# Kernel tuning notes

Measured on AMD Instinct MI355X. Metric: run time of the kernel, lower is better.

## Reference

```python
import jax, jax.numpy as jnp
import numpy as np

DIM = 768
NUM_HEADS = 12
HEAD_DIM = DIM // NUM_HEADS
SCALE = HEAD_DIM ** -0.5
RPB_HIDDEN = 64


def setup_inputs() -> dict:
    key = jax.random.key(0)
    ks = jax.random.split(key, 7)
    B, N, C = 8, 1024, DIM
    x = jax.random.normal(ks[0], (B, N, C), dtype=jnp.float32)
    qkv_w = jax.random.normal(ks[1], (3 * C, C), dtype=jnp.float32) * (C ** -0.5)
    proj_w = jax.random.normal(ks[2], (C, C), dtype=jnp.float32) * (C ** -0.5)
    proj_b = jnp.zeros((C,), dtype=jnp.float32)
    rpb_w1 = jax.random.normal(ks[3], (RPB_HIDDEN, 2), dtype=jnp.float32) * 0.5
    rpb_b1 = jax.random.normal(ks[4], (RPB_HIDDEN,), dtype=jnp.float32) * 0.1
    rpb_w2 = jax.random.normal(ks[5], (NUM_HEADS, RPB_HIDDEN), dtype=jnp.float32) * 0.1
    rpb_b2 = jax.random.normal(ks[6], (NUM_HEADS,), dtype=jnp.float32) * 0.1
    return {"x": x, "qkv_w": qkv_w, "proj_w": proj_w, "proj_b": proj_b,
            "rpb_w1": rpb_w1, "rpb_b1": rpb_b1, "rpb_w2": rpb_w2, "rpb_b2": rpb_b2}


def _relative_position_bias(N, w1, b1, w2, b2):
    # grid coords: x varies fastest, y varies slowest (perfect-square N assumed)
    g = int(N ** 0.5)
    c = jnp.arange(g, dtype=jnp.float32)
    cx = jnp.tile(c, g)                      # [N]
    cy = jnp.repeat(c, g)                    # [N]
    rel_x = cx[:, None] - cx[None, :]        # [N, N]
    rel_y = cy[:, None] - cy[None, :]        # [N, N]
    rel = jnp.stack([rel_x, rel_y], axis=-1) # [N, N, 2]
    h = jax.nn.relu(jnp.einsum('nmk,hk->nmh', rel, w1) + b1)    # [N, N, hidden]
    bias = jnp.einsum('nmk,hk->nmh', h, w2) + b2                # [N, N, H]
    return jnp.transpose(bias, (2, 0, 1))                       # [H, N, N]


def reference(x, qkv_w, proj_w, proj_b, rpb_w1, rpb_b1, rpb_w2, rpb_b2):
    B, N, C = x.shape
    H, D = NUM_HEADS, HEAD_DIM
    qkv = jnp.einsum('bnc,oc->bno', x, qkv_w)            # [B, N, 3C]
    qkv = qkv.reshape(B, N, 3, H, D).transpose(2, 0, 3, 1, 4)  # [3, B, H, N, D]
    q, k, v = qkv[0], qkv[1], qkv[2]
    attn = jnp.einsum('bhnd,bhmd->bhnm', q, k) * SCALE   # [B, H, N, N]
    bias = _relative_position_bias(N, rpb_w1, rpb_b1, rpb_w2, rpb_b2)
    attn = attn + bias[None]                              # broadcast over batch
    attn = jax.nn.softmax(attn, axis=-1)
    out = jnp.einsum('bhnm,bhmd->bhnd', attn, v)         # [B, H, N, D]
    out = out.transpose(0, 2, 1, 3).reshape(B, N, C)
    return jnp.einsum('bnc,oc->bno', out, proj_w) + proj_b
```

## Files before the change

### kernel.cpp

```cpp
#include <hip/hip_runtime.h>

#define C_DIM 768
#define NHEADS 12
#define HDIM 64
#define BATCH 8
#define SEQ 1024
#define SCALE_F 0.125f
#define TBL 3969
#define BTSL 2079

typedef float f32x4 __attribute__((ext_vector_type(4)));
typedef short s16x4 __attribute__((ext_vector_type(4)));
typedef short s16x8 __attribute__((ext_vector_type(8)));
typedef unsigned int u32x2 __attribute__((ext_vector_type(2)));

__device__ inline unsigned short f2bf(float f) {
    unsigned r;
    asm("v_cvt_pk_bf16_f32 %0, %1, %2" : "=v"(r) : "v"(f), "v"(f));
    return (unsigned short)r;
}
__device__ inline unsigned cvtpk(float lo, float hi) {
    unsigned r;
    asm("v_cvt_pk_bf16_f32 %0, %1, %2" : "=v"(r) : "v"(lo), "v"(hi));
    return r;
}

#define GLOAD_LDS16(gsrc, ldst)                                                   \
    __builtin_amdgcn_global_load_lds(                                             \
        (const __attribute__((address_space(1))) unsigned int*)(gsrc),            \
        (__attribute__((address_space(3))) unsigned int*)(ldst), 16, 0, 0)


__global__ __launch_bounds__(256)
void cvt_bf16_kernel(const float* __restrict__ in, unsigned short* __restrict__ out,
                     int n8)
{
    int i = blockIdx.x * 256 + threadIdx.x;
    if (i >= n8) return;
    const float4* p = (const float4*)in + (size_t)i * 2;
    float4 a = p[0], b = p[1];
    s16x8 v;
    v[0] = (short)f2bf(a.x); v[1] = (short)f2bf(a.y);
    v[2] = (short)f2bf(a.z); v[3] = (short)f2bf(a.w);
    v[4] = (short)f2bf(b.x); v[5] = (short)f2bf(b.y);
    v[6] = (short)f2bf(b.z); v[7] = (short)f2bf(b.w);
    *((s16x8*)out + i) = v;
}


#define MFMA_SWAP(aa, bb)                                          \
    _Pragma("unroll") for (int i_ = 0; i_ < 4; ++i_)               \
    _Pragma("unroll") for (int j_ = 0; j_ < 4; ++j_)               \
        acc[i_][j_] = __builtin_amdgcn_mfma_f32_16x16x32_bf16(     \
            bb[j_], aa[i_], acc[i_][j_], 0, 0, 0);

#define MFMA_NORM(aa, bb)                                          \
    _Pragma("unroll") for (int i_ = 0; i_ < 4; ++i_)               \
    _Pragma("unroll") for (int j_ = 0; j_ < 4; ++j_)               \
        acc[i_][j_] = __builtin_amdgcn_mfma_f32_16x16x32_bf16(     \
            aa[i_], bb[j_], acc[i_][j_], 0, 0, 0);

#define STG_HALF(buf, kt, half)                                                    \
    GLOAD_LDS16(Ab + ((size_t)(m0 + w * 32 + (half) * 16 + srow8) * 768 +          \
                (kt) * 64) * 2 + sch8 * 16, &Al[buf][w * 32 + (half) * 16][0]);    \
    GLOAD_LDS16(Ab + ((size_t)(m0 + w * 32 + (half) * 16 + 8 + srow8) * 768 +      \
                (kt) * 64) * 2 + sch8 * 16, &Al[buf][w * 32 + (half) * 16 + 8][0]);\
    GLOAD_LDS16(Wb + ((size_t)(n0 + w * 16 + (half) * 8 + srow8) * 768 +           \
                (kt) * 64) * 2 + sch8 * 16, &Bl[buf][w * 16 + (half) * 8][0]);

#define PHASE_READS(cur, s, ar, br)                                                \
    _Pragma("unroll") for (int i_ = 0; i_ < 4; ++i_) {                             \
        ar[i_] = *(const s16x8*)((const char*)&Al[cur][wr * 64 + i_ * 16 + l15][0] \
                 + ((((s) * 4 + lhi) ^ (l15 & 7)) * 16));                          \
        br[i_] = *(const s16x8*)((const char*)&Bl[cur][wc * 64 + i_ * 16 + l15][0] \
                 + ((((s) * 4 + lhi) ^ (l15 & 7)) * 16));                          \
    }

__global__ __launch_bounds__(512)
void gemm_qkv_mfma(const unsigned short* __restrict__ A,
                   const unsigned short* __restrict__ W,
                   unsigned short* __restrict__ qo, unsigned short* __restrict__ ko,
                   unsigned short* __restrict__ vto)
{
    __shared__ unsigned short Al[2][256][64];
    __shared__ unsigned short Bl[2][128][64];

    const int b0 = blockIdx.x;
    const int sw = (b0 & 7) * 72 + (b0 >> 3);
    const int bx = sw % 18, by = sw / 18;
    const int m0 = by * 256;
    const int n0 = bx * 128;
    const int lane = threadIdx.x & 63, w = threadIdx.x >> 6;
    const int wr = w >> 1, wc = w & 1;
    const int l15 = lane & 15, lhi = lane >> 4;

    const int which = n0 / 768;
    const int ncol0 = n0 - which * 768;

    const int srow8 = lane >> 3;
    const int sch8  = (lane & 7) ^ srow8;

    f32x4 acc[4][4];
#pragma unroll
    for (int i = 0; i < 4; ++i)
#pragma unroll
        for (int j = 0; j < 4; ++j)
            acc[i][j] = (f32x4){0.f, 0.f, 0.f, 0.f};

    const char* Ab = (const char*)A;
    const char* Wb = (const char*)W;

    STG_HALF(0, 0, 0)
    STG_HALF(0, 0, 1)

    for (int kt = 0; kt < 12; ++kt) {
        const int cur = kt & 1;
        if (kt + 1 < 12) {
            STG_HALF(cur ^ 1, kt + 1, 0)
            asm volatile("s_waitcnt vmcnt(3)" ::: "memory");
        } else {
            asm volatile("s_waitcnt vmcnt(0)" ::: "memory");
        }
        __builtin_amdgcn_s_barrier();

        {
            s16x8 ar[4], br[4];
            PHASE_READS(cur, 0, ar, br)
            if (kt + 1 < 12) { STG_HALF(cur ^ 1, kt + 1, 1) }
            asm volatile("s_waitcnt lgkmcnt(0)" ::: "memory");
            __builtin_amdgcn_sched_barrier(0);
            __builtin_amdgcn_s_setprio(1);
            if (which < 2) { MFMA_SWAP(ar, br) } else { MFMA_NORM(ar, br) }
            __builtin_amdgcn_s_setprio(0);
        }
        __builtin_amdgcn_s_barrier();

        {
            s16x8 ar[4], br[4];
            PHASE_READS(cur, 1, ar, br)
            asm volatile("s_waitcnt lgkmcnt(0)" ::: "memory");
            __builtin_amdgcn_sched_barrier(0);
            __builtin_amdgcn_s_setprio(1);
            if (which < 2) { MFMA_SWAP(ar, br) } else { MFMA_NORM(ar, br) }
            __builtin_amdgcn_s_setprio(0);
        }
        __builtin_amdgcn_s_barrier();
    }

    const int h = (ncol0 >> 6) + wc;
    if (which < 2) {
        unsigned short* dst0 = (which == 0) ? qo : ko;
#pragma unroll
        for (int i = 0; i < 4; ++i) {
            int mm = m0 + wr * 64 + i * 16 + l15;
            int b_ = mm >> 10, nn = mm & 1023;
            unsigned short* rowp = dst0 + (((size_t)(b_ * NHEADS + h) * SEQ + nn) << 6);
#pragma unroll
            for (int j = 0; j < 4; ++j) {
                s16x4 v;
#pragma unroll
                for (int r = 0; r < 4; ++r) v[r] = (short)f2bf(acc[i][j][r]);
                *(s16x4*)(rowp + j * 16 + lhi * 4) = v;
            }
        }
    } else {
#pragma unroll
        for (int i = 0; i < 4; ++i) {
            int mm0 = m0 + wr * 64 + i * 16 + lhi * 4;
            int b_ = mm0 >> 10, nn0 = mm0 & 1023;
#pragma unroll
            for (int j = 0; j < 4; ++j) {
                int d = j * 16 + l15;
                s16x4 v;
#pragma unroll
                for (int r = 0; r < 4; ++r) v[r] = (short)f2bf(acc[i][j][r]);
                *(s16x4*)(vto + (((size_t)(b_ * NHEADS + h) * HDIM + d) << 10) + nn0) = v;
            }
        }
    }
}

__global__ __launch_bounds__(512)
void gemm_proj_mfma(const unsigned short* __restrict__ A,
                    const unsigned short* __restrict__ W,
                    const float* __restrict__ pb, float* __restrict__ out)
{
    __shared__ unsigned short Al[2][256][64];
    __shared__ unsigned short Bl[2][128][64];

    const int b0 = blockIdx.x;
    const int sw = (b0 & 7) * 24 + (b0 >> 3);
    const int bx = sw % 6, by = sw / 6;
    const int m0 = by * 256;
    const int n0 = bx * 128;
    const int lane = threadIdx.x & 63, w = threadIdx.x >> 6;
    const int wr = w >> 1, wc = w & 1;
    const int l15 = lane & 15, lhi = lane >> 4;

    const int srow8 = lane >> 3;
    const int sch8  = (lane & 7) ^ srow8;

    f32x4 acc[4][4];
#pragma unroll
    for (int i = 0; i < 4; ++i)
#pragma unroll
        for (int j = 0; j < 4; ++j)
            acc[i][j] = (f32x4){0.f, 0.f, 0.f, 0.f};

    const char* Ab = (const char*)A;
    const char* Wb = (const char*)W;

    STG_HALF(0, 0, 0)
    STG_HALF(0, 0, 1)

    for (int kt = 0; kt < 12; ++kt) {
        const int cur = kt & 1;
        if (kt + 1 < 12) {
            STG_HALF(cur ^ 1, kt + 1, 0)
            asm volatile("s_waitcnt vmcnt(3)" ::: "memory");
        } else {
            asm volatile("s_waitcnt vmcnt(0)" ::: "memory");
        }
        __builtin_amdgcn_s_barrier();

        {
            s16x8 ar[4], br[4];
            PHASE_READS(cur, 0, ar, br)
            if (kt + 1 < 12) { STG_HALF(cur ^ 1, kt + 1, 1) }
            asm volatile("s_waitcnt lgkmcnt(0)" ::: "memory");
            __builtin_amdgcn_sched_barrier(0);
            __builtin_amdgcn_s_setprio(1);
            MFMA_SWAP(ar, br)
            __builtin_amdgcn_s_setprio(0);
        }
        __builtin_amdgcn_s_barrier();

        {
            s16x8 ar[4], br[4];
            PHASE_READS(cur, 1, ar, br)
            asm volatile("s_waitcnt lgkmcnt(0)" ::: "memory");
            __builtin_amdgcn_sched_barrier(0);
            __builtin_amdgcn_s_setprio(1);
            MFMA_SWAP(ar, br)
            __builtin_amdgcn_s_setprio(0);
        }
        __builtin_amdgcn_s_barrier();
    }

    float4 bias[4];
#pragma unroll
    for (int j = 0; j < 4; ++j)
        bias[j] = *(const float4*)&pb[n0 + wc * 64 + j * 16 + lhi * 4];
#pragma unroll
    for (int i = 0; i < 4; ++i) {
        int mm = m0 + wr * 64 + i * 16 + l15;
        float* rowp = out + (size_t)mm * C_DIM + n0 + wc * 64;
#pragma unroll
        for (int j = 0; j < 4; ++j) {
            float4 o = {acc[i][j][0] + bias[j].x, acc[i][j][1] + bias[j].y,
                        acc[i][j][2] + bias[j].z, acc[i][j][3] + bias[j].w};
            *(float4*)(rowp + j * 16 + lhi * 4) = o;
        }
    }
}

__global__ __launch_bounds__(256)
void rpb_table_kernel(const float* __restrict__ w1, const float* __restrict__ b1,
                      const float* __restrict__ w2, const float* __restrict__ b2,
                      float* __restrict__ btab)
{
    int t = blockIdx.x * 256 + threadIdx.x;
    if (t >= TBL) return;
    float dy = (float)(t / 63 - 31);
    float dx = (float)(t % 63 - 31);
    float acc[NHEADS];
#pragma unroll
    for (int h = 0; h < NHEADS; ++h) acc[h] = b2[h];
    for (int j = 0; j < 64; ++j) {
        float hj = fmaf(w1[j * 2], dx, fmaf(w1[j * 2 + 1], dy, b1[j]));
        hj = fmaxf(hj, 0.f);
#pragma unroll
        for (int h = 0; h < NHEADS; ++h) acc[h] = fmaf(w2[h * 64 + j], hj, acc[h]);
    }
#pragma unroll
    for (int h = 0; h < NHEADS; ++h) btab[h * TBL + t] = acc[h];
}

__global__ __launch_bounds__(256)
void attn_mfma_kernel(const unsigned short* __restrict__ qb,
                      const unsigned short* __restrict__ kb,
                      const unsigned short* __restrict__ vtb,
                      const float* __restrict__ btab,
                      unsigned short* __restrict__ out)
{
    __shared__ unsigned short Klds[2][64][64];
    __shared__ unsigned short Vlds[2][64][64];
    __shared__ unsigned short Plds[4][16][72];
    __shared__ float bt[BTSL];

    const int d0 = blockIdx.x;
    const int idx = d0 >> 3;
    const int qblk = idx & 15;
    const int hb = (idx >> 4) * 8 + (d0 & 7);
    const int h = hb % NHEADS, b = hb / NHEADS;

    const int n0 = qblk * 64;
    const int ny0 = n0 >> 5;
    const int t = threadIdx.x;
    const int lane = t & 63, w = t >> 6;
    const int l15 = lane & 15, lhi = lane >> 4;

    const size_t headND = ((size_t)(b * NHEADS + h)) * SEQ * HDIM;
    const char* qg = (const char*)(qb + headND);
    const char* kg = (const char*)(kb + headND);
    const char* vg = (const char*)(vtb + headND);

    s16x8 qf0, qf1;
    {
        const char* qrow = qg + (size_t)(n0 + w * 16 + l15) * 128;
        qf0 = *(const s16x8*)(qrow + lhi * 16);
        qf1 = *(const s16x8*)(qrow + 64 + lhi * 16);
    }
    {
        const int btbase = h * TBL + ny0 * 63;
        for (int i = t; i < BTSL; i += 256) bt[i] = btab[btbase + i];
    }

    int bidx[4][4];
    {
        const int nq = n0 + w * 16 + l15;
#pragma unroll
        for (int n = 0; n < 4; ++n)
#pragma unroll
            for (int r = 0; r < 4; ++r) {
                int koff = n * 16 + lhi * 4 + r;
                int dyl = (nq >> 5) - ny0 - (koff >> 5) + 31;
                int dx = (nq & 31) - (koff & 31) + 31;
                bidx[n][r] = dyl * 63 + dx;
            }
    }

    f32x4 of[4];
    float m_i = -1e30f, l_i = 0.f;
#pragma unroll
    for (int n = 0; n < 4; ++n) of[n] = (f32x4){0.f, 0.f, 0.f, 0.f};

    const int srow = (lane >> 3);
    const int sch  = (lane & 7);

    asm volatile("s_waitcnt vmcnt(0)" ::: "memory");
#pragma unroll
    for (int p = 0; p < 2; ++p) {
        int row = w * 16 + p * 8 + srow;
        int chk = sch ^ (row & 7);
        GLOAD_LDS16(kg + (size_t)row * 128 + chk * 16, &Klds[0][w * 16 + p * 8][0]);
        GLOAD_LDS16(vg + (size_t)row * 2048 + chk * 16, &Vlds[0][w * 16 + p * 8][0]);
    }
    asm volatile("s_waitcnt lgkmcnt(0)" ::: "memory");
    __builtin_amdgcn_s_barrier();

    int boff = 0;
    for (int kt = 0; kt < 16; ++kt) {
        const int cur = kt & 1;
        if (kt + 1 < 16) {
            const int c1 = (kt + 1) * 64;
#pragma unroll
            for (int p = 0; p < 2; ++p) {
                int row = w * 16 + p * 8 + srow;
                int chk = sch ^ (row & 7);
                GLOAD_LDS16(kg + (size_t)(c1 + row) * 128 + chk * 16,
                            &Klds[cur ^ 1][w * 16 + p * 8][0]);
                GLOAD_LDS16(vg + (size_t)row * 2048 + c1 * 2 + chk * 16,
                            &Vlds[cur ^ 1][w * 16 + p * 8][0]);
            }
            asm volatile("s_waitcnt vmcnt(4)" ::: "memory");
        } else {
            asm volatile("s_waitcnt vmcnt(0)" ::: "memory");
        }
        __builtin_amdgcn_s_barrier();

        f32x4 sf[4];
#pragma unroll
        for (int n = 0; n < 4; ++n) {
            int key = 16 * n + l15;
            const char* krow = (const char*)&Klds[cur][key][0];
            s16x8 kf0 = *(const s16x8*)(krow + ((lhi     ^ (key & 7)) * 16));
            s16x8 kf1 = *(const s16x8*)(krow + (((4+lhi) ^ (key & 7)) * 16));
            f32x4 z = (f32x4){0.f, 0.f, 0.f, 0.f};
            sf[n] = __builtin_amdgcn_mfma_f32_16x16x32_bf16(kf0, qf0, z, 0, 0, 0);
            sf[n] = __builtin_amdgcn_mfma_f32_16x16x32_bf16(kf1, qf1, sf[n], 0, 0, 0);
        }

        float s_[4][4];
        float mx = -1e30f;
#pragma unroll
        for (int n = 0; n < 4; ++n)
#pragma unroll
            for (int r = 0; r < 4; ++r) {
                s_[n][r] = fmaf(sf[n][r], SCALE_F, bt[bidx[n][r] + boff]);
                mx = fmaxf(mx, s_[n][r]);
            }
        mx = fmaxf(mx, __shfl_xor(mx, 16));
        mx = fmaxf(mx, __shfl_xor(mx, 32));
        if (__any(mx > m_i + 8.f)) {
            float mn = fmaxf(m_i, mx);
            float sc = __expf(m_i - mn);
            m_i = mn;
            l_i *= sc;
#pragma unroll
            for (int r = 0; r < 4; ++r) {
                float scr = __shfl(sc, lhi * 4 + r);
#pragma unroll
                for (int n = 0; n < 4; ++n) of[n][r] *= scr;
            }
        }
        float p_[4][4];
        float rs = 0.f;
#pragma unroll
        for (int n = 0; n < 4; ++n)
#pragma unroll
            for (int r = 0; r < 4; ++r) {
                p_[n][r] = __expf(s_[n][r] - m_i);
                rs += p_[n][r];
            }
        rs += __shfl_xor(rs, 16);
        rs += __shfl_xor(rs, 32);
        l_i += rs;
#pragma unroll
        for (int n = 0; n < 4; ++n) {
            u32x2 pw;
            pw[0] = cvtpk(p_[n][0], p_[n][1]);
            pw[1] = cvtpk(p_[n][2], p_[n][3]);
            *(u32x2*)&Plds[w][l15][n * 16 + lhi * 4] = pw;
        }
        boff -= 126;
        asm volatile("s_waitcnt lgkmcnt(0)" ::: "memory");
        __builtin_amdgcn_sched_barrier(0);

#pragma unroll
        for (int kwin = 0; kwin < 2; ++kwin) {
            s16x8 pa = *(const s16x8*)&Plds[w][l15][kwin * 32 + lhi * 8];
#pragma unroll
            for (int n = 0; n < 4; ++n) {
                int d  = 16 * n + l15;
                int cd = kwin * 4 + lhi;
                const char* vrow = (const char*)&Vlds[cur][d][0];
                s16x8 vf = *(const s16x8*)(vrow + ((cd ^ (d & 7)) * 16));
                of[n] = __builtin_amdgcn_mfma_f32_16x16x32_bf16(pa, vf, of[n], 0, 0, 0);
            }
        }
        asm volatile("s_waitcnt lgkmcnt(0)" ::: "memory");
        __builtin_amdgcn_s_barrier();
    }

    float inv = 1.f / l_i;
#pragma unroll
    for (int r = 0; r < 4; ++r) {
        float invr = __shfl(inv, lhi * 4 + r);
        int nq = n0 + w * 16 + lhi * 4 + r;
        unsigned short* orow = out + ((size_t)b * SEQ + nq) * C_DIM + h * 64;
#pragma unroll
        for (int n = 0; n < 4; ++n)
            orow[16 * n + l15] = f2bf(of[n][r] * invr);
    }
}

extern "C" void kernel_launch(void* const* d_in, const int* in_sizes, int n_in,
                              void* d_out, int out_size, void* d_ws, size_t ws_size,
                              hipStream_t stream) {
    const float* x      = (const float*)d_in[0];
    const float* qkv_w  = (const float*)d_in[1];
    const float* proj_w = (const float*)d_in[2];
    const float* proj_b = (const float*)d_in[3];
    const float* rpb_w1 = (const float*)d_in[4];
    const float* rpb_b1 = (const float*)d_in[5];
    const float* rpb_w2 = (const float*)d_in[6];
    const float* rpb_b2 = (const float*)d_in[7];
    float* out = (float*)d_out;

    char* wsb = (char*)d_ws;
    unsigned short* qbuf    = (unsigned short*)(wsb);
    unsigned short* kbuf    = (unsigned short*)(wsb + 12582912);
    unsigned short* vtbuf   = (unsigned short*)(wsb + 25165824);
    unsigned short* abuf    = (unsigned short*)(wsb + 37748736);
    float*          btab    = (float*)         (wsb + 50331648);
    unsigned short* xbf     = (unsigned short*)(wsb + 50522160);
    unsigned short* qkvwbf  = (unsigned short*)(wsb + 63105072);
    unsigned short* projwbf = (unsigned short*)(wsb + 66644016);

    cvt_bf16_kernel<<<dim3(786432 / 256), dim3(256), 0, stream>>>(x, xbf, 786432);
    cvt_bf16_kernel<<<dim3(864), dim3(256), 0, stream>>>(qkv_w, qkvwbf, 221184);
    cvt_bf16_kernel<<<dim3(288), dim3(256), 0, stream>>>(proj_w, projwbf, 73728);

    rpb_table_kernel<<<dim3((TBL + 255) / 256), dim3(256), 0, stream>>>(
        rpb_w1, rpb_b1, rpb_w2, rpb_b2, btab);

    gemm_qkv_mfma<<<dim3(576), dim3(512), 0, stream>>>(
        xbf, qkvwbf, qbuf, kbuf, vtbuf);

    attn_mfma_kernel<<<dim3(1536), dim3(256), 0, stream>>>(
        qbuf, kbuf, vtbuf, btab, abuf);

    gemm_proj_mfma<<<dim3(192), dim3(512), 0, stream>>>(
        abuf, projwbf, proj_b, out);
}
```

Before: 172.9 us.

## Enlarge attention query tile to 256 rows with 8 waves, two groups each

The attention kernel now runs 512-thread blocks that each cover 256 query rows. Every wave handles two 16-row query groups against the same K/V tiles, so each LDS K/V load feeds twice the MFMA work and total K/V global traffic drops by four. The bias indexing is simplified using the 32-wide grid structure, and the bias slice in LDS grows to match. The grid shrinks from 1536 to 384 blocks, which risks lower occupancy and uneven load across CUs, and per-thread register use roughly doubles.

```diff
diff --git a/kernel.cpp b/kernel.cpp
--- a/kernel.cpp
+++ b/kernel.cpp
@@ -7,7 +7,7 @@
 #define SEQ 1024
 #define SCALE_F 0.125f
 #define TBL 3969
-#define BTSL 2079
+#define BTSL2 2457
 
 typedef float f32x4 __attribute__((ext_vector_type(4)));
 typedef short s16x4 __attribute__((ext_vector_type(4)));
@@ -47,7 +47,6 @@
     *((s16x8*)out + i) = v;
 }
 
-
 #define MFMA_SWAP(aa, bb)                                          \
     _Pragma("unroll") for (int i_ = 0; i_ < 4; ++i_)               \
     _Pragma("unroll") for (int j_ = 0; j_ < 4; ++j_)               \
@@ -286,7 +285,7 @@
     for (int h = 0; h < NHEADS; ++h) btab[h * TBL + t] = acc[h];
 }
 
-__global__ __launch_bounds__(256)
+__global__ __launch_bounds__(512)
 void attn_mfma_kernel(const unsigned short* __restrict__ qb,
                       const unsigned short* __restrict__ kb,
                       const unsigned short* __restrict__ vtb,
@@ -295,17 +294,17 @@
 {
     __shared__ unsigned short Klds[2][64][64];
     __shared__ unsigned short Vlds[2][64][64];
-    __shared__ unsigned short Plds[4][16][72];
-    __shared__ float bt[BTSL];
+    __shared__ unsigned short Plds[8][2][16][72];
+    __shared__ float bt[BTSL2];
 
     const int d0 = blockIdx.x;
+    const int xcd = d0 & 7;
     const int idx = d0 >> 3;
-    const int qblk = idx & 15;
-    const int hb = (idx >> 4) * 8 + (d0 & 7);
+    const int qblk = idx & 3;
+    const int hb = (idx >> 2) * 8 + xcd;
     const int h = hb % NHEADS, b = hb / NHEADS;
 
-    const int n0 = qblk * 64;
-    const int ny0 = n0 >> 5;
+    const int n0 = qblk * 256;
     const int t = threadIdx.x;
     const int lane = t & 63, w = t >> 6;
     const int l15 = lane & 15, lhi = lane >> 4;
@@ -315,47 +314,40 @@
     const char* kg = (const char*)(kb + headND);
     const char* vg = (const char*)(vtb + headND);
 
-    s16x8 qf0, qf1;
+    s16x8 qf[2][2];
+#pragma unroll
+    for (int g = 0; g < 2; ++g) {
+        const char* qrow = qg + (size_t)(n0 + w * 32 + g * 16 + l15) * 128;
+        qf[g][0] = *(const s16x8*)(qrow + lhi * 16);
+        qf[g][1] = *(const s16x8*)(qrow + 64 + lhi * 16);
+    }
     {
-        const char* qrow = qg + (size_t)(n0 + w * 16 + l15) * 128;
-        qf0 = *(const s16x8*)(qrow + lhi * 16);
-        qf1 = *(const s16x8*)(qrow + 64 + lhi * 16);
-    }
-    {
-        const int btbase = h * TBL + ny0 * 63;
-        for (int i = t; i < BTSL; i += 256) bt[i] = btab[btbase + i];
-    }
-
-    int bidx[4][4];
-    {
-        const int nq = n0 + w * 16 + l15;
-#pragma unroll
-        for (int n = 0; n < 4; ++n)
-#pragma unroll
-            for (int r = 0; r < 4; ++r) {
-                int koff = n * 16 + lhi * 4 + r;
-                int dyl = (nq >> 5) - ny0 - (koff >> 5) + 31;
-                int dx = (nq & 31) - (koff & 31) + 31;
-                bidx[n][r] = dyl * 63 + dx;
-            }
-    }
-
-    f32x4 of[4];
-    float m_i = -1e30f, l_i = 0.f;
-#pragma unroll
-    for (int n = 0; n < 4; ++n) of[n] = (f32x4){0.f, 0.f, 0.f, 0.f};
-
-    const int srow = (lane >> 3);
-    const int sch  = (lane & 7);
+        const int btbase = h * TBL + (n0 >> 5) * 63;
+        for (int i = t; i < BTSL2; i += 512) bt[i] = btab[btbase + i];
+    }
+
+    int bidx0[4];
+#pragma unroll
+    for (int n = 0; n < 4; ++n) {
+        int koff = n * 16 + lhi * 4;
+        int dyl = w - (koff >> 5) + 31;
+        int dx = l15 - (koff & 31) + 31;
+        bidx0[n] = dyl * 63 + dx;
+    }
+
+    f32x4 of[2][4];
+    float m_i[2] = {-1e30f, -1e30f}, l_i[2] = {0.f, 0.f};
+#pragma unroll
+    for (int g = 0; g < 2; ++g)
+#pragma unroll
+        for (int n = 0; n < 4; ++n) of[g][n] = (f32x4){0.f, 0.f, 0.f, 0.f};
+
+    const int krow = w * 8 + (lane >> 3);
+    const int chk  = (lane & 7) ^ (krow & 7);
 
     asm volatile("s_waitcnt vmcnt(0)" ::: "memory");
-#pragma unroll
-    for (int p = 0; p < 2; ++p) {
-        int row = w * 16 + p * 8 + srow;
-        int chk = sch ^ (row & 7);
-        GLOAD_LDS16(kg + (size_t)row * 128 + chk * 16, &Klds[0][w * 16 + p * 8][0]);
-        GLOAD_LDS16(vg + (size_t)row * 2048 + chk * 16, &Vlds[0][w * 16 + p * 8][0]);
-    }
+    GLOAD_LDS16(kg + (size_t)krow * 128 + chk * 16, &Klds[0][w * 8][0]);
+    GLOAD_LDS16(vg + (size_t)krow * 2048 + chk * 16, &Vlds[0][w * 8][0]);
     asm volatile("s_waitcnt lgkmcnt(0)" ::: "memory");
     __builtin_amdgcn_s_barrier();
 
@@ -364,74 +356,73 @@
         const int cur = kt & 1;
         if (kt + 1 < 16) {
             const int c1 = (kt + 1) * 64;
-#pragma unroll
-            for (int p = 0; p < 2; ++p) {
-                int row = w * 16 + p * 8 + srow;
-                int chk = sch ^ (row & 7);
-                GLOAD_LDS16(kg + (size_t)(c1 + row) * 128 + chk * 16,
-                            &Klds[cur ^ 1][w * 16 + p * 8][0]);
-                GLOAD_LDS16(vg + (size_t)row * 2048 + c1 * 2 + chk * 16,
-                            &Vlds[cur ^ 1][w * 16 + p * 8][0]);
-            }
-            asm volatile("s_waitcnt vmcnt(4)" ::: "memory");
+            GLOAD_LDS16(kg + (size_t)(c1 + krow) * 128 + chk * 16,
+                        &Klds[cur ^ 1][w * 8][0]);
+            GLOAD_LDS16(vg + (size_t)krow * 2048 + c1 * 2 + chk * 16,
+                        &Vlds[cur ^ 1][w * 8][0]);
+            asm volatile("s_waitcnt vmcnt(2)" ::: "memory");
         } else {
             asm volatile("s_waitcnt vmcnt(0)" ::: "memory");
         }
         __builtin_amdgcn_s_barrier();
 
-        f32x4 sf[4];
+        f32x4 sf[2][4];
 #pragma unroll
         for (int n = 0; n < 4; ++n) {
             int key = 16 * n + l15;
-            const char* krow = (const char*)&Klds[cur][key][0];
-            s16x8 kf0 = *(const s16x8*)(krow + ((lhi     ^ (key & 7)) * 16));
-            s16x8 kf1 = *(const s16x8*)(krow + (((4+lhi) ^ (key & 7)) * 16));
+            const char* krp = (const char*)&Klds[cur][key][0];
+            s16x8 kf0 = *(const s16x8*)(krp + ((lhi     ^ (key & 7)) * 16));
+            s16x8 kf1 = *(const s16x8*)(krp + (((4+lhi) ^ (key & 7)) * 16));
             f32x4 z = (f32x4){0.f, 0.f, 0.f, 0.f};
-            sf[n] = __builtin_amdgcn_mfma_f32_16x16x32_bf16(kf0, qf0, z, 0, 0, 0);
-            sf[n] = __builtin_amdgcn_mfma_f32_16x16x32_bf16(kf1, qf1, sf[n], 0, 0, 0);
-        }
-
-        float s_[4][4];
-        float mx = -1e30f;
-#pragma unroll
-        for (int n = 0; n < 4; ++n)
-#pragma unroll
-            for (int r = 0; r < 4; ++r) {
-                s_[n][r] = fmaf(sf[n][r], SCALE_F, bt[bidx[n][r] + boff]);
-                mx = fmaxf(mx, s_[n][r]);
+            sf[0][n] = __builtin_amdgcn_mfma_f32_16x16x32_bf16(kf0, qf[0][0], z, 0, 0, 0);
+            sf[0][n] = __builtin_amdgcn_mfma_f32_16x16x32_bf16(kf1, qf[0][1], sf[0][n], 0, 0, 0);
+            sf[1][n] = __builtin_amdgcn_mfma_f32_16x16x32_bf16(kf0, qf[1][0], z, 0, 0, 0);
+            sf[1][n] = __builtin_amdgcn_mfma_f32_16x16x32_bf16(kf1, qf[1][1], sf[1][n], 0, 0, 0);
+        }
+
+#pragma unroll
+        for (int g = 0; g < 2; ++g) {
+            const int gb = g * 16;
+            float s_[4][4];
+            float mx = -1e30f;
+#pragma unroll
+            for (int n = 0; n < 4; ++n)
+#pragma unroll
+                for (int r = 0; r < 4; ++r) {
+                    s_[n][r] = fmaf(sf[g][n][r], SCALE_F,
+                                    bt[bidx0[n] - r + gb + boff]);
+                    mx = fmaxf(mx, s_[n][r]);
+                }
+            mx = fmaxf(mx, __shfl_xor(mx, 16));
+            mx = fmaxf(mx, __shfl_xor(mx, 32));
+            if (__any(mx > m_i[g] + 8.f)) {
+                float mn = fmaxf(m_i[g], mx);
+                float sc = __expf(m_i[g] - mn);
+                m_i[g] = mn;
+                l_i[g] *= sc;
+#pragma unroll
+                for (int r = 0; r < 4; ++r) {
+                    float scr = __shfl(sc, lhi * 4 + r);
+#pragma unroll
+                    for (int n = 0; n < 4; ++n) of[g][n][r] *= scr;
+                }
             }
-        mx = fmaxf(mx, __shfl_xor(mx, 16));
-        mx = fmaxf(mx, __shfl_xor(mx, 32));
-        if (__any(mx > m_i + 8.f)) {
-            float mn = fmaxf(m_i, mx);
-            float sc = __expf(m_i - mn);
-            m_i = mn;
-            l_i *= sc;
-#pragma unroll
-            for (int r = 0; r < 4; ++r) {
-                float scr = __shfl(sc, lhi * 4 + r);
-#pragma unroll
-                for (int n = 0; n < 4; ++n) of[n][r] *= scr;
+            float rs = 0.f;
+#pragma unroll
+            for (int n = 0; n < 4; ++n) {
+                float p0 = __expf(s_[n][0] - m_i[g]);
+                float p1 = __expf(s_[n][1] - m_i[g]);
+                float p2 = __expf(s_[n][2] - m_i[g]);
+                float p3 = __expf(s_[n][3] - m_i[g]);
+                rs += (p0 + p1) + (p2 + p3);
+                u32x2 pw;
+                pw[0] = cvtpk(p0, p1);
+                pw[1] = cvtpk(p2, p3);
+                *(u32x2*)&Plds[w][g][l15][n * 16 + lhi * 4] = pw;
             }
-        }
-        float p_[4][4];
-        float rs = 0.f;
-#pragma unroll
-        for (int n = 0; n < 4; ++n)
-#pragma unroll
-            for (int r = 0; r < 4; ++r) {
-                p_[n][r] = __expf(s_[n][r] - m_i);
-                rs += p_[n][r];
-            }
-        rs += __shfl_xor(rs, 16);
-        rs += __shfl_xor(rs, 32);
-        l_i += rs;
-#pragma unroll
-        for (int n = 0; n < 4; ++n) {
-            u32x2 pw;
-            pw[0] = cvtpk(p_[n][0], p_[n][1]);
-            pw[1] = cvtpk(p_[n][2], p_[n][3]);
-            *(u32x2*)&Plds[w][l15][n * 16 + lhi * 4] = pw;
+            rs += __shfl_xor(rs, 16);
+            rs += __shfl_xor(rs, 32);
+            l_i[g] += rs;
         }
         boff -= 126;
         asm volatile("s_waitcnt lgkmcnt(0)" ::: "memory");
@@ -439,29 +430,34 @@
 
 #pragma unroll
         for (int kwin = 0; kwin < 2; ++kwin) {
-            s16x8 pa = *(const s16x8*)&Plds[w][l15][kwin * 32 + lhi * 8];
+            s16x8 pa0 = *(const s16x8*)&Plds[w][0][l15][kwin * 32 + lhi * 8];
+            s16x8 pa1 = *(const s16x8*)&Plds[w][1][l15][kwin * 32 + lhi * 8];
 #pragma unroll
             for (int n = 0; n < 4; ++n) {
                 int d  = 16 * n + l15;
                 int cd = kwin * 4 + lhi;
                 const char* vrow = (const char*)&Vlds[cur][d][0];
                 s16x8 vf = *(const s16x8*)(vrow + ((cd ^ (d & 7)) * 16));
-                of[n] = __builtin_amdgcn_mfma_f32_16x16x32_bf16(pa, vf, of[n], 0, 0, 0);
+                of[0][n] = __builtin_amdgcn_mfma_f32_16x16x32_bf16(pa0, vf, of[0][n], 0, 0, 0);
+                of[1][n] = __builtin_amdgcn_mfma_f32_16x16x32_bf16(pa1, vf, of[1][n], 0, 0, 0);
             }
         }
         asm volatile("s_waitcnt lgkmcnt(0)" ::: "memory");
         __builtin_amdgcn_s_barrier();
     }
 
-    float inv = 1.f / l_i;
-#pragma unroll
-    for (int r = 0; r < 4; ++r) {
-        float invr = __shfl(inv, lhi * 4 + r);
-        int nq = n0 + w * 16 + lhi * 4 + r;
-        unsigned short* orow = out + ((size_t)b * SEQ + nq) * C_DIM + h * 64;
-#pragma unroll
-        for (int n = 0; n < 4; ++n)
-            orow[16 * n + l15] = f2bf(of[n][r] * invr);
+#pragma unroll
+    for (int g = 0; g < 2; ++g) {
+        float inv = 1.f / l_i[g];
+#pragma unroll
+        for (int r = 0; r < 4; ++r) {
+            float invr = __shfl(inv, lhi * 4 + r);
+            int nq = n0 + w * 32 + g * 16 + lhi * 4 + r;
+            unsigned short* orow = out + ((size_t)b * SEQ + nq) * C_DIM + h * 64;
+#pragma unroll
+            for (int n = 0; n < 4; ++n)
+                orow[16 * n + l15] = f2bf(of[g][n][r] * invr);
+        }
     }
 }
 
@@ -498,7 +494,7 @@
     gemm_qkv_mfma<<<dim3(576), dim3(512), 0, stream>>>(
         xbf, qkvwbf, qbuf, kbuf, vtbuf);
 
-    attn_mfma_kernel<<<dim3(1536), dim3(256), 0, stream>>>(
+    attn_mfma_kernel<<<dim3(384), dim3(512), 0, stream>>>(
         qbuf, kbuf, vtbuf, btab, abuf);
 
     gemm_proj_mfma<<<dim3(192), dim3(512), 0, stream>>>(
```

Measured after the change: 166.7 us. -3.6%, faster.
